# Kernel tuning notes

Measured on AMD Instinct MI355X. Metric: run time of the kernel, lower is better.

The kernel has to match this reference:

```python
import jax, jax.numpy as jnp
import numpy as np

N, E = 40000, 640000
IN_DIM, EDGE_DIM, HID, H1 = 5, 11, 128, 4
NEG_SLOPE = 0.2


def _add_self_loops(ei, ea, n):
    # PyG GATConv default: add_self_loops=True, fill_value='mean' for edge_attr
    loop = jnp.arange(n, dtype=ei.dtype)
    ei2 = jnp.concatenate([ei, jnp.stack([loop, loop])], axis=1)
    ea2 = jnp.concatenate([ea, jnp.broadcast_to(ea.mean(0), (n, ea.shape[1]))], axis=0)
    return ei2, ea2


def _gat(x, ei, ea, W, We, a_src, a_dst, a_edge, b, H, C):
    # Single GATConv layer (eval mode, dropout inactive)
    n = x.shape[0]
    xh = (x @ W).reshape(n, H, C)            # [N,H,C]
    eh = (ea @ We).reshape(-1, H, C)         # [E,H,C]
    src, dst = ei[0], ei[1]
    a_s = (xh * a_src).sum(-1)               # [N,H]
    a_d = (xh * a_dst).sum(-1)               # [N,H]
    alpha = jax.nn.leaky_relu(a_s[src] + a_d[dst] + (eh * a_edge).sum(-1), NEG_SLOPE)  # [E,H]
    amax = jax.ops.segment_max(alpha, dst, num_segments=n)
    ex = jnp.exp(alpha - amax[dst])
    den = jax.ops.segment_sum(ex, dst, num_segments=n)
    w = ex / (den[dst] + 1e-16)              # softmax over inbound edges per dst
    out = jax.ops.segment_sum(xh[src] * w[:, :, None], dst, num_segments=n)  # [N,H,C]
    return out.reshape(n, H * C) + b


def setup_inputs() -> dict:
    key = jax.random.key(0)
    ks = jax.random.split(key, 20)
    s = 0.1
    return {
        "x": jax.random.normal(ks[0], (N, IN_DIM), jnp.float32),
        "edge_index": jax.random.randint(ks[1], (2, E), 0, N),
        "edge_attr": jax.random.normal(ks[2], (E, EDGE_DIM), jnp.float32),
        "W1": jax.random.normal(ks[3], (IN_DIM, H1 * HID), jnp.float32) * s,
        "We1": jax.random.normal(ks[4], (EDGE_DIM, H1 * HID), jnp.float32) * s,
        "a_src1": jax.random.normal(ks[5], (H1, HID), jnp.float32) * s,
        "a_dst1": jax.random.normal(ks[6], (H1, HID), jnp.float32) * s,
        "a_edge1": jax.random.normal(ks[7], (H1, HID), jnp.float32) * s,
        "b1": jnp.zeros((H1 * HID,), jnp.float32),
        # layer 2 (512 -> 128, 1 head)
        "W2": jax.random.normal(ks[8], (H1 * HID, HID), jnp.float32) * s,
        "We2": jax.random.normal(ks[9], (EDGE_DIM, HID), jnp.float32) * s,
        "a_src2": jax.random.normal(ks[10], (1, HID), jnp.float32) * s,
        "a_dst2": jax.random.normal(ks[11], (1, HID), jnp.float32) * s,
        "a_edge2": jax.random.normal(ks[12], (1, HID), jnp.float32) * s,
        "b2": jnp.zeros((HID,), jnp.float32),
        # final linear 128 -> 1
        "Wfc": jax.random.normal(ks[13], (HID, 1), jnp.float32) * s,
        "bfc": jnp.zeros((1,), jnp.float32),
    }


def reference(x, edge_index, edge_attr,
              W1, We1, a_src1, a_dst1, a_edge1, b1,
              W2, We2, a_src2, a_dst2, a_edge2, b2,
              Wfc, bfc):
    ei, ea = _add_self_loops(edge_index, edge_attr, x.shape[0])
    h = jax.nn.relu(_gat(x, ei, ea, W1, We1, a_src1, a_dst1, a_edge1, b1, H1, HID))
    h = jax.nn.relu(_gat(h, ei, ea, W2, We2, a_src2, a_dst2, a_edge2, b2, 1, HID))
    return jax.nn.sigmoid(h @ Wfc + bfc)
```

## Files before the change

### kernel.cpp

```cpp
#include <hip/hip_runtime.h>

#define NN   40000
#define EE   640000
#define EE2  680000
#define IND  5
#define ED   11
#define HIDD 128
#define F1   512
#define NBW  10000

typedef unsigned short u16;
typedef unsigned int   u32;
typedef __attribute__((ext_vector_type(8))) short bf16x8;
typedef __attribute__((ext_vector_type(4))) float f32x4;

__device__ __forceinline__ float bf2f(u16 u) { return __uint_as_float(((u32)u) << 16); }
__device__ __forceinline__ u16 f2bf(float f) {
    u32 u = __float_as_uint(f);
    return (u16)((u + 0x7FFFu + ((u >> 16) & 1u)) >> 16);
}

__device__ __forceinline__ float wsum(float v) {
#pragma unroll
    for (int o = 32; o; o >>= 1) v += __shfl_xor(v, o, 64);
    return v;
}
__device__ __forceinline__ float lrelu(float v) { return v > 0.f ? v : 0.2f * v; }


__global__ void k_init(float* __restrict__ consts, int* __restrict__ counts) {
    int i = blockIdx.x * blockDim.x + threadIdx.x;
    if (i < 256) consts[i] = 0.f;
    if (i < NN) counts[i] = 0;
}

__global__ void k_constsA(float* __restrict__ consts,
                          const float* __restrict__ We1, const float* __restrict__ ae1,
                          const float* __restrict__ We2, const float* __restrict__ ae2) {
    int t = threadIdx.x;
    if (t < 44) {
        int k = t >> 2, h = t & 3;
        float s = 0.f;
        for (int c = 0; c < HIDD; ++c)
            s += We1[k * F1 + h * HIDD + c] * ae1[h * HIDD + c];
        consts[16 + t] = s;
    }
    if (t >= 48 && t < 48 + ED) {
        int k = t - 48;
        float s = 0.f;
        for (int c = 0; c < HIDD; ++c)
            s += We2[k * HIDD + c] * ae2[c];
        consts[64 + k] = s;
    }
}

__global__ void k_wswz(const float* __restrict__ W2, u16* __restrict__ bsw) {
    int t = blockIdx.x * blockDim.x + threadIdx.x;
    if (t >= 8192) return;
    int lane = t & 63, ks = (t >> 6) & 15, nt = t >> 10;
    int kbase = ks * 32 + (lane >> 4) * 8;
    int n = nt * 16 + (lane & 15);
    size_t dst = (size_t)t * 8;
#pragma unroll
    for (int j = 0; j < 8; ++j)
        bsw[dst + j] = f2bf(W2[(size_t)(kbase + j) * HIDD + n]);
}

__global__ void k_count(const int* __restrict__ ei, int* __restrict__ counts,
                        int* __restrict__ rank) {
    int i = blockIdx.x * blockDim.x + threadIdx.x;
    if (i >= EE) return;
    rank[i] = atomicAdd(&counts[ei[EE + i]], 1);
}

#define SBLK 256
#define SGRID ((NN + SBLK - 1) / SBLK)
__global__ void __launch_bounds__(SBLK) k_scanA(const int* __restrict__ counts,
                                                int* __restrict__ local_ex,
                                                int* __restrict__ bsum) {
    __shared__ int sh[SBLK];
    int t = threadIdx.x;
    int i = blockIdx.x * SBLK + t;
    int v = (i < NN) ? counts[i] + 1 : 0;
    sh[t] = v;
    __syncthreads();
    for (int o = 1; o < SBLK; o <<= 1) {
        int u = (t >= o) ? sh[t - o] : 0;
        __syncthreads();
        sh[t] += u;
        __syncthreads();
    }
    if (i < NN) local_ex[i] = sh[t] - v;
    if (t == SBLK - 1) bsum[blockIdx.x] = sh[t];
}

__global__ void __launch_bounds__(SBLK) k_scanB(int* __restrict__ bsum,
                                                int* __restrict__ boff) {
    __shared__ int sh[SBLK];
    int t = threadIdx.x;
    int v = (t < SGRID) ? bsum[t] : 0;
    sh[t] = v;
    __syncthreads();
    for (int o = 1; o < SBLK; o <<= 1) {
        int u = (t >= o) ? sh[t - o] : 0;
        __syncthreads();
        sh[t] += u;
        __syncthreads();
    }
    if (t < SGRID) boff[t] = sh[t] - v;
}

__global__ void __launch_bounds__(SBLK) k_scanC(const int* __restrict__ local_ex,
                                                const int* __restrict__ boff,
                                                int* __restrict__ row_off) {
    int t = threadIdx.x;
    int i = blockIdx.x * SBLK + t;
    if (i < NN) row_off[i] = local_ex[i] + boff[blockIdx.x];
    if (i == 0) row_off[NN] = EE2;
}

__global__ void __launch_bounds__(256) k_build(const float* __restrict__ ea,
                                               const int* __restrict__ ei,
                                               const int* __restrict__ rank,
                                               const int* __restrict__ row_off,
                                               const float* __restrict__ consts,
                                               uint4* __restrict__ rec,
                                               float* __restrict__ psum) {
    int i = blockIdx.x * 256 + threadIdx.x;
    int s = ei[i];
    int d = ei[EE + i];
    int pos = row_off[d] + rank[i];
    const float* row = ea + (size_t)i * ED;
    float r[ED];
#pragma unroll
    for (int k = 0; k < ED; ++k) r[k] = row[k];
    float e0 = 0.f, e1 = 0.f, e2 = 0.f, e3 = 0.f, et = 0.f;
#pragma unroll
    for (int k = 0; k < ED; ++k) {
        float a = r[k];
        e0 += a * consts[16 + k * 4 + 0];
        e1 += a * consts[16 + k * 4 + 1];
        e2 += a * consts[16 + k * 4 + 2];
        e3 += a * consts[16 + k * 4 + 3];
        et += a * consts[64 + k];
    }
    uint4 q;
    q.x = (u32)f2bf(e0) | ((u32)f2bf(e1) << 16);
    q.y = (u32)f2bf(e2) | ((u32)f2bf(e3) << 16);
    q.z = (u32)s;
    q.w = __float_as_uint(et);
    rec[pos] = q;
#pragma unroll
    for (int k = 0; k < ED; ++k) r[k] = wsum(r[k]);
    int wgid = blockIdx.x * 4 + (threadIdx.x >> 6);
    int lane = threadIdx.x & 63;
    if (lane < ED) psum[wgid * ED + lane] = r[lane];
}

__global__ void __launch_bounds__(256) k_sumred(const float* __restrict__ psum,
                                                float* __restrict__ consts) {
    __shared__ float sh[256];
    __shared__ float mean[ED];
    int t = threadIdx.x;
    float acc[ED];
#pragma unroll
    for (int k = 0; k < ED; ++k) acc[k] = 0.f;
    for (int w = t; w < NBW; w += 256) {
        const float* p = psum + (size_t)w * ED;
#pragma unroll
        for (int k = 0; k < ED; ++k) acc[k] += p[k];
    }
    for (int k = 0; k < ED; ++k) {
        sh[t] = acc[k];
        __syncthreads();
        for (int o = 128; o; o >>= 1) {
            if (t < o) sh[t] += sh[t + o];
            __syncthreads();
        }
        if (t == 0) {
            float m = sh[0] * (1.0f / (float)EE);
            mean[k] = m;
            consts[k] = m;
        }
        __syncthreads();
    }
    if (t < 4) {
        float s = 0.f;
        for (int k = 0; k < ED; ++k) s += mean[k] * consts[16 + k * 4 + t];
        consts[80 + t] = s;
    }
    if (t == 8) {
        float s = 0.f;
        for (int k = 0; k < ED; ++k) s += mean[k] * consts[64 + k];
        consts[96] = s;
    }
}

__global__ void k_self(const int* __restrict__ row_off, const int* __restrict__ counts,
                       const float* __restrict__ consts, uint4* __restrict__ rec) {
    int n = blockIdx.x * blockDim.x + threadIdx.x;
    if (n >= NN) return;
    int pos = row_off[n] + counts[n];
    uint4 q;
    q.x = (u32)f2bf(consts[80]) | ((u32)f2bf(consts[81]) << 16);
    q.y = (u32)f2bf(consts[82]) | ((u32)f2bf(consts[83]) << 16);
    q.z = (u32)n;
    q.w = __float_as_uint(consts[96]);
    rec[pos] = q;
}

__global__ void __launch_bounds__(64) k_xh1(const float* __restrict__ x,
                                            const float* __restrict__ W1,
                                            const float* __restrict__ as1,
                                            const float* __restrict__ ad1,
                                            float* __restrict__ aS1,
                                            float* __restrict__ aD1) {
    int n = blockIdx.x, t = threadIdx.x;
    int c0 = t * 8, h = t >> 4;
    const float* xp = x + (size_t)n * IND;
    float x0 = xp[0], x1 = xp[1], x2 = xp[2], x3 = xp[3], x4 = xp[4];
    float p = 0.f, q = 0.f;
#pragma unroll
    for (int j = 0; j < 8; ++j) {
        int c = c0 + j;
        float v = x0 * W1[0 * F1 + c] + x1 * W1[1 * F1 + c] + x2 * W1[2 * F1 + c]
                + x3 * W1[3 * F1 + c] + x4 * W1[4 * F1 + c];
        p += v * as1[c];
        q += v * ad1[c];
    }
#pragma unroll
    for (int o = 1; o <= 8; o <<= 1) {
        p += __shfl_xor(p, o, 64);
        q += __shfl_xor(q, o, 64);
    }
    if ((t & 15) == 0) {
        aS1[n * 4 + h] = p;
        aD1[n * 4 + h] = q;
    }
}

__global__ void __launch_bounds__(64) k_agg1(const int* __restrict__ row_off,
                                             const uint4* __restrict__ rec,
                                             const float* __restrict__ aS1,
                                             const float* __restrict__ aD1,
                                             const float* __restrict__ x,
                                             const float* __restrict__ W1,
                                             const float* __restrict__ b1,
                                             u16* __restrict__ h1) {
    int n = blockIdx.x, t = threadIdx.x;
    int s0 = row_off[n], s1 = row_off[n + 1];
    int h = t & 3;
    float4 adv = *(const float4*)(aD1 + (size_t)n * 4);
    float adh = (h == 0) ? adv.x : (h == 1) ? adv.y : (h == 2) ? adv.z : adv.w;
    float z = 0.f, xa0 = 0.f, xa1 = 0.f, xa2 = 0.f, xa3 = 0.f, xa4 = 0.f;
    for (int i = s0 + (t >> 2); i < s1; i += 16) {
        uint4 q = rec[i];
        u32 w2 = (h & 2) ? q.y : q.x;
        float eh = bf2f((h & 1) ? (u16)(w2 >> 16) : (u16)(w2 & 0xFFFF));
        int s = (int)q.z;
        float a = lrelu(eh + aS1[(size_t)s * 4 + h] + adh);
        float ex = __expf(a);
        z += ex;
        const float* xp = x + (size_t)s * IND;
        xa0 += ex * xp[0]; xa1 += ex * xp[1]; xa2 += ex * xp[2];
        xa3 += ex * xp[3]; xa4 += ex * xp[4];
    }
#pragma unroll
    for (int o = 4; o <= 32; o <<= 1) {
        z   += __shfl_xor(z, o, 64);
        xa0 += __shfl_xor(xa0, o, 64); xa1 += __shfl_xor(xa1, o, 64);
        xa2 += __shfl_xor(xa2, o, 64); xa3 += __shfl_xor(xa3, o, 64);
        xa4 += __shfl_xor(xa4, o, 64);
    }
    int ho = t >> 4;
    float zz = __shfl(z, ho);
    float y0 = __shfl(xa0, ho), y1 = __shfl(xa1, ho), y2 = __shfl(xa2, ho);
    float y3 = __shfl(xa3, ho), y4 = __shfl(xa4, ho);
    float ih = 1.f / (zz + 1e-16f);
    int c0 = t * 8;
#pragma unroll
    for (int j = 0; j < 8; ++j) {
        int c = c0 + j;
        float v = (y0 * W1[0 * F1 + c] + y1 * W1[1 * F1 + c] + y2 * W1[2 * F1 + c]
                 + y3 * W1[3 * F1 + c] + y4 * W1[4 * F1 + c]) * ih;
        h1[(size_t)n * F1 + c] = f2bf(fmaxf(v + b1[c], 0.f));
    }
}

__global__ void __launch_bounds__(256, 2) k_gemm2(const u16* __restrict__ h1,
                                                  const u16* __restrict__ bsw,
                                                  const float* __restrict__ as2,
                                                  const float* __restrict__ ad2,
                                                  u16* __restrict__ xh2,
                                                  float* __restrict__ aS2,
                                                  float* __restrict__ aD2) {
    int tid = threadIdx.x;
    int wv = tid >> 6, lane = tid & 63;
    int tile = blockIdx.x * 4 + wv;
    if (tile >= 2500) return;
    int n0 = tile * 16;
    int mrow = lane & 15, quad = lane >> 4;
    const u16* aptr = h1 + (size_t)(n0 + mrow) * F1 + quad * 8;
    const u16* bbase = bsw + lane * 8;
    f32x4 acc[8];
#pragma unroll
    for (int nt = 0; nt < 8; ++nt) acc[nt] = (f32x4){0.f, 0.f, 0.f, 0.f};

    bf16x8 b0[8], b1v[8];
    bf16x8 af0, af1;
    af0 = *(const bf16x8*)(aptr);
#pragma unroll
    for (int nt = 0; nt < 8; ++nt)
        b0[nt] = *(const bf16x8*)(bbase + nt * 8192);
#pragma unroll
    for (int ks = 0; ks < 16; ++ks) {
        if (ks < 15) {
            af1 = *(const bf16x8*)(aptr + (ks + 1) * 32);
#pragma unroll
            for (int nt = 0; nt < 8; ++nt)
                b1v[nt] = *(const bf16x8*)(bbase + nt * 8192 + (ks + 1) * 512);
        }
#pragma unroll
        for (int nt = 0; nt < 8; ++nt)
            acc[nt] = __builtin_amdgcn_mfma_f32_16x16x32_bf16(af0, b0[nt], acc[nt], 0, 0, 0);
        af0 = af1;
#pragma unroll
        for (int nt = 0; nt < 8; ++nt) b0[nt] = b1v[nt];
    }
    float ps[4] = {0.f, 0.f, 0.f, 0.f}, pd[4] = {0.f, 0.f, 0.f, 0.f};
#pragma unroll
    for (int nt = 0; nt < 8; ++nt) {
        int col = nt * 16 + mrow;
        float sa = as2[col], da = ad2[col];
#pragma unroll
        for (int r = 0; r < 4; ++r) {
            float v = acc[nt][r];
            xh2[(size_t)(n0 + quad * 4 + r) * HIDD + col] = f2bf(v);
            ps[r] += v * sa; pd[r] += v * da;
        }
    }
#pragma unroll
    for (int r = 0; r < 4; ++r) {
#pragma unroll
        for (int o = 1; o <= 8; o <<= 1) {
            ps[r] += __shfl_xor(ps[r], o, 64);
            pd[r] += __shfl_xor(pd[r], o, 64);
        }
        if (mrow == 0) {
            aS2[n0 + quad * 4 + r] = ps[r];
            aD2[n0 + quad * 4 + r] = pd[r];
        }
    }
}

__global__ void __launch_bounds__(64) k_agg2(const int* __restrict__ row_off,
                                             const uint4* __restrict__ rec,
                                             const float* __restrict__ aS2,
                                             const float* __restrict__ aD2,
                                             const u16* __restrict__ xh2,
                                             const float* __restrict__ bias2,
                                             const float* __restrict__ Wfc,
                                             const float* __restrict__ bfc,
                                             float* __restrict__ out) {
    int n = blockIdx.x, t = threadIdx.x;
    int s0 = row_off[n], s1 = row_off[n + 1];
    float adn = aD2[n];
    int g = t >> 4, l = t & 15;
    int c0 = l * 8;
    float z = 0.f;
    float acc[8];
#pragma unroll
    for (int j = 0; j < 8; ++j) acc[j] = 0.f;
    for (int i = s0 + g; i < s1; i += 4) {
        uint4 qe = rec[i];
        int s = (int)qe.z;
        float et2 = __uint_as_float(qe.w);
        float ex = __expf(lrelu(aS2[s] + adn + et2));
        z += ex;
        uint4 q = *(const uint4*)(xh2 + (size_t)s * HIDD + c0);
        acc[0] += ex * bf2f((u16)(q.x & 0xFFFF)); acc[1] += ex * bf2f((u16)(q.x >> 16));
        acc[2] += ex * bf2f((u16)(q.y & 0xFFFF)); acc[3] += ex * bf2f((u16)(q.y >> 16));
        acc[4] += ex * bf2f((u16)(q.z & 0xFFFF)); acc[5] += ex * bf2f((u16)(q.z >> 16));
        acc[6] += ex * bf2f((u16)(q.w & 0xFFFF)); acc[7] += ex * bf2f((u16)(q.w >> 16));
    }
#pragma unroll
    for (int o = 16; o <= 32; o <<= 1) {
        z += __shfl_xor(z, o, 64);
#pragma unroll
        for (int j = 0; j < 8; ++j) acc[j] += __shfl_xor(acc[j], o, 64);
    }
    float inv = 1.f / (z + 1e-16f);
    float p = 0.f;
#pragma unroll
    for (int j = 0; j < 8; ++j) {
        float o = fmaxf(acc[j] * inv + bias2[c0 + j], 0.f);
        p += o * Wfc[c0 + j];
    }
#pragma unroll
    for (int o = 1; o <= 8; o <<= 1) p += __shfl_xor(p, o, 64);
    if (t == 0) {
        float logit = p + bfc[0];
        out[n] = 1.f / (1.f + __expf(-logit));
    }
}

extern "C" void kernel_launch(void* const* d_in, const int* in_sizes, int n_in,
                              void* d_out, int out_size, void* d_ws, size_t ws_size,
                              hipStream_t stream) {
    (void)in_sizes; (void)n_in; (void)out_size; (void)ws_size;
    const float* x   = (const float*)d_in[0];
    const int*   ei  = (const int*)d_in[1];
    const float* ea  = (const float*)d_in[2];
    const float* W1  = (const float*)d_in[3];
    const float* We1 = (const float*)d_in[4];
    const float* as1 = (const float*)d_in[5];
    const float* ad1 = (const float*)d_in[6];
    const float* ae1 = (const float*)d_in[7];
    const float* b1  = (const float*)d_in[8];
    const float* W2  = (const float*)d_in[9];
    const float* We2 = (const float*)d_in[10];
    const float* as2 = (const float*)d_in[11];
    const float* ad2 = (const float*)d_in[12];
    const float* ae2 = (const float*)d_in[13];
    const float* b2v = (const float*)d_in[14];
    const float* Wfc = (const float*)d_in[15];
    const float* bfc = (const float*)d_in[16];
    float* out = (float*)d_out;

    char* ws = (char*)d_ws;
    size_t off = 0;
    auto take = [&](size_t nb) {
        size_t r = off;
        off += (nb + 255) & ~(size_t)255;
        return r;
    };
    float* consts = (float*)(ws + take(1024));
    int* row_off  = (int*)(ws + take((size_t)(NN + 1) * 4));
    int* counts   = (int*)(ws + take((size_t)NN * 4));
    int* local_ex = (int*)(ws + take((size_t)NN * 4));
    int* bsum     = (int*)(ws + take(1024));
    int* boff     = (int*)(ws + take(1024));
    int* rank     = (int*)(ws + take((size_t)EE * 4));
    float* psum   = (float*)(ws + take((size_t)NBW * ED * 4));
    uint4* rec    = (uint4*)(ws + take((size_t)EE2 * 16));
    float* aS1    = (float*)(ws + take((size_t)NN * 16));
    float* aD1    = (float*)(ws + take((size_t)NN * 16));
    float* aS2    = (float*)(ws + take((size_t)NN * 4));
    float* aD2    = (float*)(ws + take((size_t)NN * 4));
    u16* h1       = (u16*)(ws + take((size_t)NN * F1 * 2));
    u16* xh2      = (u16*)(ws + take((size_t)NN * HIDD * 2));
    u16* w2b      = (u16*)(ws + take((size_t)65536 * 2));

    k_init<<<(NN + 255) / 256, 256, 0, stream>>>(consts, counts);
    k_constsA<<<1, 64, 0, stream>>>(consts, We1, ae1, We2, ae2);
    k_wswz<<<32, 256, 0, stream>>>(W2, w2b);
    k_count<<<(EE + 255) / 256, 256, 0, stream>>>(ei, counts, rank);
    k_scanA<<<SGRID, SBLK, 0, stream>>>(counts, local_ex, bsum);
    k_scanB<<<1, SBLK, 0, stream>>>(bsum, boff);
    k_scanC<<<SGRID, SBLK, 0, stream>>>(local_ex, boff, row_off);

    k_build<<<EE / 256, 256, 0, stream>>>(ea, ei, rank, row_off, consts, rec, psum);
    k_sumred<<<1, 256, 0, stream>>>(psum, consts);
    k_self<<<(NN + 255) / 256, 256, 0, stream>>>(row_off, counts, consts, rec);

    k_xh1<<<NN, 64, 0, stream>>>(x, W1, as1, ad1, aS1, aD1);
    k_agg1<<<NN, 64, 0, stream>>>(row_off, rec, aS1, aD1, x, W1, b1, h1);

    k_gemm2<<<625, 256, 0, stream>>>(h1, w2b, as2, ad2, xh2, aS2, aD2);
    k_agg2<<<NN, 64, 0, stream>>>(row_off, rec, aS2, aD2, xh2, b2v, Wfc, bfc, out);
}
```

Before: 282.1 us.

## Fuse prep kernels, handle self-loops inline, and pack four nodes per block

Merges the init, constants, W2 swizzle and layer-1 attention-score kernels into one multi-role prep launch, and folds the scanB pass into scanC. Self-loop records are no longer written into the CSR; each aggregation kernel adds the self-loop term directly. The build kernel reduces its per-wave partial sums in shared memory, which shrinks the sumred input, and both aggregation kernels now run four node-waves per 256-thread block. The aim is fewer launches, less record traffic and fewer tiny blocks, at the cost of more branchy kernels and a per-block redundant block-offset reduction in scanC.

```diff
diff --git a/kernel.cpp b/kernel.cpp
--- a/kernel.cpp
+++ b/kernel.cpp
@@ -2,12 +2,11 @@
 
 #define NN   40000
 #define EE   640000
-#define EE2  680000
 #define IND  5
 #define ED   11
 #define HIDD 128
 #define F1   512
-#define NBW  10000
+#define PSB  2500
 
 typedef unsigned short u16;
 typedef unsigned int   u32;
@@ -28,42 +27,83 @@
 __device__ __forceinline__ float lrelu(float v) { return v > 0.f ? v : 0.2f * v; }
 
 
-__global__ void k_init(float* __restrict__ consts, int* __restrict__ counts) {
-    int i = blockIdx.x * blockDim.x + threadIdx.x;
-    if (i < 256) consts[i] = 0.f;
-    if (i < NN) counts[i] = 0;
-}
-
-__global__ void k_constsA(float* __restrict__ consts,
-                          const float* __restrict__ We1, const float* __restrict__ ae1,
-                          const float* __restrict__ We2, const float* __restrict__ ae2) {
-    int t = threadIdx.x;
-    if (t < 44) {
-        int k = t >> 2, h = t & 3;
-        float s = 0.f;
-        for (int c = 0; c < HIDD; ++c)
-            s += We1[k * F1 + h * HIDD + c] * ae1[h * HIDD + c];
-        consts[16 + t] = s;
-    }
-    if (t >= 48 && t < 48 + ED) {
-        int k = t - 48;
-        float s = 0.f;
-        for (int c = 0; c < HIDD; ++c)
-            s += We2[k * HIDD + c] * ae2[c];
-        consts[64 + k] = s;
-    }
-}
-
-__global__ void k_wswz(const float* __restrict__ W2, u16* __restrict__ bsw) {
-    int t = blockIdx.x * blockDim.x + threadIdx.x;
-    if (t >= 8192) return;
-    int lane = t & 63, ks = (t >> 6) & 15, nt = t >> 10;
-    int kbase = ks * 32 + (lane >> 4) * 8;
-    int n = nt * 16 + (lane & 15);
-    size_t dst = (size_t)t * 8;
-#pragma unroll
-    for (int j = 0; j < 8; ++j)
-        bsw[dst + j] = f2bf(W2[(size_t)(kbase + j) * HIDD + n]);
+
+#define SBLK 256
+#define SGRID ((NN + SBLK - 1) / SBLK)
+#define PREPG (SGRID + 33 + NN / 4)
+
+__global__ void __launch_bounds__(256) k_prep(int* __restrict__ counts,
+                                              float* __restrict__ consts,
+                                              const float* __restrict__ We1,
+                                              const float* __restrict__ ae1,
+                                              const float* __restrict__ We2,
+                                              const float* __restrict__ ae2,
+                                              const float* __restrict__ W2,
+                                              u16* __restrict__ bsw,
+                                              const float* __restrict__ x,
+                                              const float* __restrict__ W1,
+                                              const float* __restrict__ as1,
+                                              const float* __restrict__ ad1,
+                                              float* __restrict__ aS1,
+                                              float* __restrict__ aD1) {
+    int bid = blockIdx.x, t = threadIdx.x;
+    if (bid < SGRID) {
+        int i = bid * 256 + t;
+        if (i < NN) counts[i] = 0;
+        return;
+    }
+    if (bid == SGRID) {
+        if (t < 44) {
+            int k = t >> 2, h = t & 3;
+            float s = 0.f;
+            for (int c = 0; c < HIDD; ++c)
+                s += We1[k * F1 + h * HIDD + c] * ae1[h * HIDD + c];
+            consts[16 + t] = s;
+        }
+        if (t >= 48 && t < 48 + ED) {
+            int k = t - 48;
+            float s = 0.f;
+            for (int c = 0; c < HIDD; ++c)
+                s += We2[k * HIDD + c] * ae2[c];
+            consts[64 + k] = s;
+        }
+        return;
+    }
+    if (bid < SGRID + 33) {
+        int t2 = (bid - (SGRID + 1)) * 256 + t;
+        if (t2 >= 8192) return;
+        int lane = t2 & 63, ks = (t2 >> 6) & 15, nt = t2 >> 10;
+        int kbase = ks * 32 + (lane >> 4) * 8;
+        int n = nt * 16 + (lane & 15);
+        size_t dst = (size_t)t2 * 8;
+#pragma unroll
+        for (int j = 0; j < 8; ++j)
+            bsw[dst + j] = f2bf(W2[(size_t)(kbase + j) * HIDD + n]);
+        return;
+    }
+    int n = (bid - (SGRID + 33)) * 4 + (t >> 6);
+    int lane = t & 63;
+    int c0 = lane * 8, h = lane >> 4;
+    const float* xp = x + (size_t)n * IND;
+    float x0 = xp[0], x1 = xp[1], x2 = xp[2], x3 = xp[3], x4 = xp[4];
+    float p = 0.f, q = 0.f;
+#pragma unroll
+    for (int j = 0; j < 8; ++j) {
+        int c = c0 + j;
+        float v = x0 * W1[0 * F1 + c] + x1 * W1[1 * F1 + c] + x2 * W1[2 * F1 + c]
+                + x3 * W1[3 * F1 + c] + x4 * W1[4 * F1 + c];
+        p += v * as1[c];
+        q += v * ad1[c];
+    }
+#pragma unroll
+    for (int o = 1; o <= 8; o <<= 1) {
+        p += __shfl_xor(p, o, 64);
+        q += __shfl_xor(q, o, 64);
+    }
+    if ((lane & 15) == 0) {
+        aS1[n * 4 + h] = p;
+        aD1[n * 4 + h] = q;
+    }
 }
 
 __global__ void k_count(const int* __restrict__ ei, int* __restrict__ counts,
@@ -73,15 +113,13 @@
     rank[i] = atomicAdd(&counts[ei[EE + i]], 1);
 }
 
-#define SBLK 256
-#define SGRID ((NN + SBLK - 1) / SBLK)
 __global__ void __launch_bounds__(SBLK) k_scanA(const int* __restrict__ counts,
                                                 int* __restrict__ local_ex,
                                                 int* __restrict__ bsum) {
     __shared__ int sh[SBLK];
     int t = threadIdx.x;
     int i = blockIdx.x * SBLK + t;
-    int v = (i < NN) ? counts[i] + 1 : 0;
+    int v = (i < NN) ? counts[i] : 0;
     sh[t] = v;
     __syncthreads();
     for (int o = 1; o < SBLK; o <<= 1) {
@@ -94,29 +132,21 @@
     if (t == SBLK - 1) bsum[blockIdx.x] = sh[t];
 }
 
-__global__ void __launch_bounds__(SBLK) k_scanB(int* __restrict__ bsum,
-                                                int* __restrict__ boff) {
+__global__ void __launch_bounds__(SBLK) k_scanC(const int* __restrict__ local_ex,
+                                                const int* __restrict__ bsum,
+                                                int* __restrict__ row_off) {
     __shared__ int sh[SBLK];
-    int t = threadIdx.x;
-    int v = (t < SGRID) ? bsum[t] : 0;
-    sh[t] = v;
+    int t = threadIdx.x, b = blockIdx.x;
+    sh[t] = (t < b && t < SGRID) ? bsum[t] : 0;
     __syncthreads();
-    for (int o = 1; o < SBLK; o <<= 1) {
-        int u = (t >= o) ? sh[t - o] : 0;
+    for (int o = 128; o; o >>= 1) {
+        if (t < o) sh[t] += sh[t + o];
         __syncthreads();
-        sh[t] += u;
-        __syncthreads();
-    }
-    if (t < SGRID) boff[t] = sh[t] - v;
-}
-
-__global__ void __launch_bounds__(SBLK) k_scanC(const int* __restrict__ local_ex,
-                                                const int* __restrict__ boff,
-                                                int* __restrict__ row_off) {
-    int t = threadIdx.x;
-    int i = blockIdx.x * SBLK + t;
-    if (i < NN) row_off[i] = local_ex[i] + boff[blockIdx.x];
-    if (i == 0) row_off[NN] = EE2;
+    }
+    int boff = sh[0];
+    int i = b * SBLK + t;
+    if (i < NN) row_off[i] = local_ex[i] + boff;
+    if (b == 0 && t == 0) row_off[NN] = EE;
 }
 
 __global__ void __launch_bounds__(256) k_build(const float* __restrict__ ea,
@@ -126,6 +156,7 @@
                                                const float* __restrict__ consts,
                                                uint4* __restrict__ rec,
                                                float* __restrict__ psum) {
+    __shared__ float sh[4 * ED];
     int i = blockIdx.x * 256 + threadIdx.x;
     int s = ei[i];
     int d = ei[EE + i];
@@ -152,38 +183,40 @@
     rec[pos] = q;
 #pragma unroll
     for (int k = 0; k < ED; ++k) r[k] = wsum(r[k]);
-    int wgid = blockIdx.x * 4 + (threadIdx.x >> 6);
-    int lane = threadIdx.x & 63;
-    if (lane < ED) psum[wgid * ED + lane] = r[lane];
+    int wv = threadIdx.x >> 6, lane = threadIdx.x & 63;
+    if (lane < ED) sh[wv * ED + lane] = r[lane];
+    __syncthreads();
+    int t = threadIdx.x;
+    if (t < ED)
+        psum[(size_t)blockIdx.x * ED + t] =
+            sh[t] + sh[ED + t] + sh[2 * ED + t] + sh[3 * ED + t];
 }
 
 __global__ void __launch_bounds__(256) k_sumred(const float* __restrict__ psum,
                                                 float* __restrict__ consts) {
-    __shared__ float sh[256];
+    __shared__ float sh[4 * ED];
     __shared__ float mean[ED];
     int t = threadIdx.x;
     float acc[ED];
 #pragma unroll
     for (int k = 0; k < ED; ++k) acc[k] = 0.f;
-    for (int w = t; w < NBW; w += 256) {
+    for (int w = t; w < PSB; w += 256) {
         const float* p = psum + (size_t)w * ED;
 #pragma unroll
         for (int k = 0; k < ED; ++k) acc[k] += p[k];
     }
-    for (int k = 0; k < ED; ++k) {
-        sh[t] = acc[k];
-        __syncthreads();
-        for (int o = 128; o; o >>= 1) {
-            if (t < o) sh[t] += sh[t + o];
-            __syncthreads();
-        }
-        if (t == 0) {
-            float m = sh[0] * (1.0f / (float)EE);
-            mean[k] = m;
-            consts[k] = m;
-        }
-        __syncthreads();
-    }
+#pragma unroll
+    for (int k = 0; k < ED; ++k) acc[k] = wsum(acc[k]);
+    int wv = t >> 6, lane = t & 63;
+    if (lane < ED) sh[wv * ED + lane] = acc[lane];
+    __syncthreads();
+    if (t < ED) {
+        float m = (sh[t] + sh[ED + t] + sh[2 * ED + t] + sh[3 * ED + t])
+                  * (1.0f / (float)EE);
+        mean[t] = m;
+        consts[t] = m;
+    }
+    __syncthreads();
     if (t < 4) {
         float s = 0.f;
         for (int k = 0; k < ED; ++k) s += mean[k] * consts[16 + k * 4 + t];
@@ -196,58 +229,17 @@
     }
 }
 
-__global__ void k_self(const int* __restrict__ row_off, const int* __restrict__ counts,
-                       const float* __restrict__ consts, uint4* __restrict__ rec) {
-    int n = blockIdx.x * blockDim.x + threadIdx.x;
-    if (n >= NN) return;
-    int pos = row_off[n] + counts[n];
-    uint4 q;
-    q.x = (u32)f2bf(consts[80]) | ((u32)f2bf(consts[81]) << 16);
-    q.y = (u32)f2bf(consts[82]) | ((u32)f2bf(consts[83]) << 16);
-    q.z = (u32)n;
-    q.w = __float_as_uint(consts[96]);
-    rec[pos] = q;
-}
-
-__global__ void __launch_bounds__(64) k_xh1(const float* __restrict__ x,
-                                            const float* __restrict__ W1,
-                                            const float* __restrict__ as1,
-                                            const float* __restrict__ ad1,
-                                            float* __restrict__ aS1,
-                                            float* __restrict__ aD1) {
-    int n = blockIdx.x, t = threadIdx.x;
-    int c0 = t * 8, h = t >> 4;
-    const float* xp = x + (size_t)n * IND;
-    float x0 = xp[0], x1 = xp[1], x2 = xp[2], x3 = xp[3], x4 = xp[4];
-    float p = 0.f, q = 0.f;
-#pragma unroll
-    for (int j = 0; j < 8; ++j) {
-        int c = c0 + j;
-        float v = x0 * W1[0 * F1 + c] + x1 * W1[1 * F1 + c] + x2 * W1[2 * F1 + c]
-                + x3 * W1[3 * F1 + c] + x4 * W1[4 * F1 + c];
-        p += v * as1[c];
-        q += v * ad1[c];
-    }
-#pragma unroll
-    for (int o = 1; o <= 8; o <<= 1) {
-        p += __shfl_xor(p, o, 64);
-        q += __shfl_xor(q, o, 64);
-    }
-    if ((t & 15) == 0) {
-        aS1[n * 4 + h] = p;
-        aD1[n * 4 + h] = q;
-    }
-}
-
-__global__ void __launch_bounds__(64) k_agg1(const int* __restrict__ row_off,
-                                             const uint4* __restrict__ rec,
-                                             const float* __restrict__ aS1,
-                                             const float* __restrict__ aD1,
-                                             const float* __restrict__ x,
-                                             const float* __restrict__ W1,
-                                             const float* __restrict__ b1,
-                                             u16* __restrict__ h1) {
-    int n = blockIdx.x, t = threadIdx.x;
+__global__ void __launch_bounds__(256) k_agg1(const int* __restrict__ row_off,
+                                              const uint4* __restrict__ rec,
+                                              const float* __restrict__ aS1,
+                                              const float* __restrict__ aD1,
+                                              const float* __restrict__ x,
+                                              const float* __restrict__ W1,
+                                              const float* __restrict__ b1,
+                                              const float* __restrict__ consts,
+                                              u16* __restrict__ h1) {
+    int n = blockIdx.x * 4 + (threadIdx.x >> 6);
+    int t = threadIdx.x & 63;
     int s0 = row_off[n], s1 = row_off[n + 1];
     int h = t & 3;
     float4 adv = *(const float4*)(aD1 + (size_t)n * 4);
@@ -265,6 +257,14 @@
         xa0 += ex * xp[0]; xa1 += ex * xp[1]; xa2 += ex * xp[2];
         xa3 += ex * xp[3]; xa4 += ex * xp[4];
     }
+    if (t < 4) {
+        float a = lrelu(consts[80 + h] + aS1[(size_t)n * 4 + h] + adh);
+        float ex = __expf(a);
+        z += ex;
+        const float* xp = x + (size_t)n * IND;
+        xa0 += ex * xp[0]; xa1 += ex * xp[1]; xa2 += ex * xp[2];
+        xa3 += ex * xp[3]; xa4 += ex * xp[4];
+    }
 #pragma unroll
     for (int o = 4; o <= 32; o <<= 1) {
         z   += __shfl_xor(z, o, 64);
@@ -353,16 +353,18 @@
     }
 }
 
-__global__ void __launch_bounds__(64) k_agg2(const int* __restrict__ row_off,
-                                             const uint4* __restrict__ rec,
-                                             const float* __restrict__ aS2,
-                                             const float* __restrict__ aD2,
-                                             const u16* __restrict__ xh2,
-                                             const float* __restrict__ bias2,
-                                             const float* __restrict__ Wfc,
-                                             const float* __restrict__ bfc,
-                                             float* __restrict__ out) {
-    int n = blockIdx.x, t = threadIdx.x;
+__global__ void __launch_bounds__(256) k_agg2(const int* __restrict__ row_off,
+                                              const uint4* __restrict__ rec,
+                                              const float* __restrict__ aS2,
+                                              const float* __restrict__ aD2,
+                                              const u16* __restrict__ xh2,
+                                              const float* __restrict__ bias2,
+                                              const float* __restrict__ Wfc,
+                                              const float* __restrict__ bfc,
+                                              const float* __restrict__ consts,
+                                              float* __restrict__ out) {
+    int n = blockIdx.x * 4 + (threadIdx.x >> 6);
+    int t = threadIdx.x & 63;
     int s0 = row_off[n], s1 = row_off[n + 1];
     float adn = aD2[n];
     int g = t >> 4, l = t & 15;
@@ -378,6 +380,15 @@
         float ex = __expf(lrelu(aS2[s] + adn + et2));
         z += ex;
         uint4 q = *(const uint4*)(xh2 + (size_t)s * HIDD + c0);
+        acc[0] += ex * bf2f((u16)(q.x & 0xFFFF)); acc[1] += ex * bf2f((u16)(q.x >> 16));
+        acc[2] += ex * bf2f((u16)(q.y & 0xFFFF)); acc[3] += ex * bf2f((u16)(q.y >> 16));
+        acc[4] += ex * bf2f((u16)(q.z & 0xFFFF)); acc[5] += ex * bf2f((u16)(q.z >> 16));
+        acc[6] += ex * bf2f((u16)(q.w & 0xFFFF)); acc[7] += ex * bf2f((u16)(q.w >> 16));
+    }
+    if (g == 0) {
+        float ex = __expf(lrelu(aS2[n] + adn + consts[96]));
+        z += ex;
+        uint4 q = *(const uint4*)(xh2 + (size_t)n * HIDD + c0);
         acc[0] += ex * bf2f((u16)(q.x & 0xFFFF)); acc[1] += ex * bf2f((u16)(q.x >> 16));
         acc[2] += ex * bf2f((u16)(q.y & 0xFFFF)); acc[3] += ex * bf2f((u16)(q.y >> 16));
         acc[4] += ex * bf2f((u16)(q.z & 0xFFFF)); acc[5] += ex * bf2f((u16)(q.z >> 16));
@@ -439,10 +450,9 @@
     int* counts   = (int*)(ws + take((size_t)NN * 4));
     int* local_ex = (int*)(ws + take((size_t)NN * 4));
     int* bsum     = (int*)(ws + take(1024));
-    int* boff     = (int*)(ws + take(1024));
     int* rank     = (int*)(ws + take((size_t)EE * 4));
-    float* psum   = (float*)(ws + take((size_t)NBW * ED * 4));
-    uint4* rec    = (uint4*)(ws + take((size_t)EE2 * 16));
+    float* psum   = (float*)(ws + take((size_t)PSB * ED * 4));
+    uint4* rec    = (uint4*)(ws + take((size_t)EE * 16));
     float* aS1    = (float*)(ws + take((size_t)NN * 16));
     float* aD1    = (float*)(ws + take((size_t)NN * 16));
     float* aS2    = (float*)(ws + take((size_t)NN * 4));
@@ -451,21 +461,15 @@
     u16* xh2      = (u16*)(ws + take((size_t)NN * HIDD * 2));
     u16* w2b      = (u16*)(ws + take((size_t)65536 * 2));
 
-    k_init<<<(NN + 255) / 256, 256, 0, stream>>>(consts, counts);
-    k_constsA<<<1, 64, 0, stream>>>(consts, We1, ae1, We2, ae2);
-    k_wswz<<<32, 256, 0, stream>>>(W2, w2b);
-    k_count<<<(EE + 255) / 256, 256, 0, stream>>>(ei, counts, rank);
+    k_prep<<<PREPG, 256, 0, stream>>>(counts, consts, We1, ae1, We2, ae2,
+                                      W2, w2b, x, W1, as1, ad1, aS1, aD1);
+    k_count<<<EE / 256, 256, 0, stream>>>(ei, counts, rank);
     k_scanA<<<SGRID, SBLK, 0, stream>>>(counts, local_ex, bsum);
-    k_scanB<<<1, SBLK, 0, stream>>>(bsum, boff);
-    k_scanC<<<SGRID, SBLK, 0, stream>>>(local_ex, boff, row_off);
-
-    k_build<<<EE / 256, 256, 0, stream>>>(ea, ei, rank, row_off, consts, rec, psum);
+    k_scanC<<<SGRID, SBLK, 0, stream>>>(local_ex, bsum, row_off);
+    k_build<<<PSB, 256, 0, stream>>>(ea, ei, rank, row_off, consts, rec, psum);
     k_sumred<<<1, 256, 0, stream>>>(psum, consts);
-    k_self<<<(NN + 255) / 256, 256, 0, stream>>>(row_off, counts, consts, rec);
-
-    k_xh1<<<NN, 64, 0, stream>>>(x, W1, as1, ad1, aS1, aD1);
-    k_agg1<<<NN, 64, 0, stream>>>(row_off, rec, aS1, aD1, x, W1, b1, h1);
-
+    k_agg1<<<NN / 4, 256, 0, stream>>>(row_off, rec, aS1, aD1, x, W1, b1, consts, h1);
     k_gemm2<<<625, 256, 0, stream>>>(h1, w2b, as2, ad2, xh2, aS2, aD2);
-    k_agg2<<<NN, 64, 0, stream>>>(row_off, rec, aS2, aD2, xh2, b2v, Wfc, bfc, out);
-}
+    k_agg2<<<NN / 4, 256, 0, stream>>>(row_off, rec, aS2, aD2, xh2, b2v, Wfc, bfc,
+                                       consts, out);
+}
```

Result: faster. 252.0 us (-10.7%).
